# Kernel tuning notes

Measured on AMD Instinct MI355X. Metric: run time of the kernel, lower is better.

The kernel has to match this reference:

```python
import jax, jax.numpy as jnp
import numpy as np

N = 100000
E = 1600000
IN_F = 16
OUT_F = 16
HEADS = 6
ALPHA_COEFF = 0.2
NEG_SLOPE = 0.2


def setup_inputs() -> dict:
    key = jax.random.key(0)
    k1, k2, k3, k4, k5, k6 = jax.random.split(key, 6)
    data = jax.random.uniform(k1, (N, IN_F), dtype=jnp.float32)
    edge_index = jax.random.randint(k2, (2, E), 0, N, dtype=jnp.int64)
    # GATConv params (glorot-ish scale)
    W = jax.random.normal(k3, (IN_F, HEADS * OUT_F), dtype=jnp.float32) * (1.0 / np.sqrt(IN_F))
    att_src = jax.random.normal(k4, (1, HEADS, OUT_F), dtype=jnp.float32) * (1.0 / np.sqrt(OUT_F))
    att_dst = jax.random.normal(k5, (1, HEADS, OUT_F), dtype=jnp.float32) * (1.0 / np.sqrt(OUT_F))
    bias = jnp.zeros((OUT_F,), dtype=jnp.float32)
    return {"data": data, "edge_index": edge_index, "W": W,
            "att_src": att_src, "att_dst": att_dst, "bias": bias}


def _gat_deformer(data, edge_index, W, att_src, att_dst, bias):
    n = data.shape[0]
    # add self loops (PyG GATConv default add_self_loops=True)
    loop = jnp.arange(n, dtype=edge_index.dtype)
    src = jnp.concatenate([edge_index[0], loop])  # [E']
    dst = jnp.concatenate([edge_index[1], loop])  # [E']

    x = (data @ W).reshape(n, HEADS, OUT_F)          # [N,H,C]
    a_src = jnp.sum(x * att_src, axis=-1)            # [N,H]
    a_dst = jnp.sum(x * att_dst, axis=-1)            # [N,H]

    e = a_src[src] + a_dst[dst]                      # [E',H]
    e = jnp.where(e > 0, e, NEG_SLOPE * e)           # leaky_relu(0.2)
    # segment softmax over destination nodes (PyG softmax, +1e-16 denom)
    seg_max = jax.ops.segment_max(e, dst, num_segments=n)
    e = jnp.exp(e - seg_max[dst])
    seg_sum = jax.ops.segment_sum(e, dst, num_segments=n)
    alpha = e / (seg_sum[dst] + 1e-16)               # [E',H]

    # first pass: weighted scatter-add of transformed features
    out = jax.ops.segment_sum(x[src] * alpha[:, :, None], dst, num_segments=n)  # [N,H,C]
    feat = out.mean(axis=1) + bias                   # concat=False -> head mean, + bias

    # second propagate: reuse (scaled) attention on raw coordinates
    coord = data[:, :2]                              # [N,2]
    alpha2 = alpha * ALPHA_COEFF                     # [E',H]
    msg = coord[src][:, None, :] * alpha2[:, :, None]  # [E',H,2]
    out_coord = jax.ops.segment_sum(msg, dst, num_segments=n).mean(axis=1)  # [N,2]

    # fix boundary nodes (masks computed from input coords)
    up = data[:, 0] == 1.0
    down = data[:, 0] == 0.0
    left = data[:, 1] == 0.0
    right = data[:, 1] == 1.0
    c0 = jnp.where(up, 1.0, jnp.where(down, 0.0, out_coord[:, 0]))
    c1 = jnp.where(right, 1.0, jnp.where(left, 0.0, out_coord[:, 1]))
    out_coord = jnp.stack([c0, c1], axis=1)

    feat = jax.nn.selu(feat)
    return out_coord, feat


def reference(data, edge_index, W, att_src, att_dst, bias):
    return _gat_deformer(data, edge_index, W, att_src, att_dst, bias)
```

## Files before the change

### kernel.cpp

```cpp
#include <hip/hip_runtime.h>
#include <hip/hip_fp16.h>
#include <math.h>

#define N_NODES 100000
#define N_EDGES 1600000
#define E_TOT (N_EDGES + N_NODES)
#define IN_FEAT 16
#define OUT_FEAT 16
#define HEADS 6
#define HF 96

#define NB 4096
#define NPB 25
#define CAP 576
#define NBLK_PART 256
#define NT_BLOCKS ((N_NODES * HEADS + 255) / 256)

__global__ void init_cursors(int* __restrict__ gcursor) {
    int b = blockIdx.x * blockDim.x + threadIdx.x;
    if (b < NB) gcursor[b] = b * CAP;
}

__global__ void prep(const int* __restrict__ esrc,
                     const int* __restrict__ edst,
                     int* __restrict__ gcursor,
                     unsigned int* __restrict__ spack,
                     const float* __restrict__ data,
                     const float* __restrict__ W,
                     const float* __restrict__ att_src,
                     const float* __restrict__ att_dst,
                     float* __restrict__ a_src,
                     float* __restrict__ a_dst,
                     unsigned short* __restrict__ data_f16) {
    __shared__ int shmem[2 * NB];

    if (blockIdx.x < NBLK_PART) {
        int* hist = shmem;
        int* base = shmem + NB;
        const int chunk = (E_TOT + NBLK_PART - 1) / NBLK_PART;
        const int e0 = blockIdx.x * chunk;
        const int e1 = min(e0 + chunk, E_TOT);

        for (int j = threadIdx.x; j < NB; j += blockDim.x) hist[j] = 0;
        __syncthreads();
        for (int e = e0 + threadIdx.x; e < e1; e += blockDim.x) {
            int d = (e < N_EDGES) ? edst[e] : (e - N_EDGES);
            atomicAdd(&hist[d / NPB], 1);
        }
        __syncthreads();
        for (int j = threadIdx.x; j < NB; j += blockDim.x) {
            int c = hist[j];
            base[j] = c ? atomicAdd(&gcursor[j], c) : 0;
        }
        __syncthreads();
        for (int j = threadIdx.x; j < NB; j += blockDim.x) hist[j] = 0;
        __syncthreads();
        for (int e = e0 + threadIdx.x; e < e1; e += blockDim.x) {
            int s, d;
            if (e < N_EDGES) { s = esrc[e]; d = edst[e]; }
            else             { s = d = e - N_EDGES; }
            int b = d / NPB;
            int r = atomicAdd(&hist[b], 1);
            int pos = base[b] + r;
            if (pos < (b + 1) * CAP)
                spack[pos] = (unsigned int)s | ((unsigned int)(d - b * NPB) << 17);
        }
    } else {
        float* sW  = (float*)shmem;
        float* sAs = sW + IN_FEAT * HF;
        float* sAd = sAs + HF;
        for (int i = threadIdx.x; i < IN_FEAT * HF; i += blockDim.x) sW[i] = W[i];
        for (int i = threadIdx.x; i < HF; i += blockDim.x) { sAs[i] = att_src[i]; sAd[i] = att_dst[i]; }
        __syncthreads();

        int gid = (blockIdx.x - NBLK_PART) * blockDim.x + threadIdx.x;
        int n = gid / HEADS;
        int h = gid % HEADS;
        if (n >= N_NODES) return;

        float dv[IN_FEAT];
        const float4* dp = (const float4*)(data + (size_t)n * IN_FEAT);
#pragma unroll
        for (int q = 0; q < 4; q++) {
            float4 v = dp[q];
            dv[q*4+0] = v.x; dv[q*4+1] = v.y; dv[q*4+2] = v.z; dv[q*4+3] = v.w;
        }

        if (h < 4) {
            unsigned int lo = (unsigned int)__half_as_ushort(__float2half_rn(dv[h*4+0]))
                            | ((unsigned int)__half_as_ushort(__float2half_rn(dv[h*4+1])) << 16);
            unsigned int hi = (unsigned int)__half_as_ushort(__float2half_rn(dv[h*4+2]))
                            | ((unsigned int)__half_as_ushort(__float2half_rn(dv[h*4+3])) << 16);
            uint2 pk; pk.x = lo; pk.y = hi;
            *(uint2*)(data_f16 + (size_t)n * IN_FEAT + h * 4) = pk;
        }

        float outv[OUT_FEAT];
#pragma unroll
        for (int fo = 0; fo < OUT_FEAT; fo++) outv[fo] = 0.f;
#pragma unroll
        for (int k = 0; k < IN_FEAT; k++) {
            float dk = dv[k];
            const float* wrow = &sW[k * HF + h * OUT_FEAT];
#pragma unroll
            for (int fo = 0; fo < OUT_FEAT; fo++) outv[fo] = fmaf(dk, wrow[fo], outv[fo]);
        }

        float as = 0.f, ad = 0.f;
#pragma unroll
        for (int fo = 0; fo < OUT_FEAT; fo++) {
            as = fmaf(outv[fo], sAs[h * OUT_FEAT + fo], as);
            ad = fmaf(outv[fo], sAd[h * OUT_FEAT + fo], ad);
        }
        a_src[n * HEADS + h] = as;
        a_dst[n * HEADS + h] = ad;
    }
}

__global__ void bucket_accumulate(const int* __restrict__ gcursor,
                                  const unsigned int* __restrict__ spack,
                                  const float* __restrict__ data,
                                  const unsigned short* __restrict__ data_f16,
                                  const float* __restrict__ a_src,
                                  const float* __restrict__ a_dst,
                                  const float* __restrict__ W,
                                  const float* __restrict__ bias,
                                  float* __restrict__ out) {
    const int b = blockIdx.x;
    const int n0 = b * NPB;
    if (n0 >= N_NODES) return;
    const int nn = min(NPB, N_NODES - n0);

    __shared__ unsigned int olist[CAP];
    __shared__ unsigned short exl[CAP * 8];
    __shared__ float wsn_l[NPB * 100];
    __shared__ int cnt[NPB];
    __shared__ int start[NPB + 1];
    __shared__ int cur[NPB];

    const int tid  = threadIdx.x;
    const int lane = tid & 63;
    const int slot = lane >> 4;
    const int f    = lane & 15;
    const int wv   = tid >> 6;

    int ecnt = gcursor[b] - b * CAP;
    if (ecnt > CAP) ecnt = CAP;

    for (int j = tid; j < NPB; j += 256) cnt[j] = 0;
    __syncthreads();
    for (int i = tid; i < ecnt; i += 256)
        atomicAdd(&cnt[spack[b * CAP + i] >> 17], 1);
    __syncthreads();
    if (tid == 0) {
        int r = 0;
        for (int j = 0; j < NPB; j++) { start[j] = r; r += cnt[j]; }
        start[NPB] = r;
    }
    __syncthreads();
    for (int j = tid; j < NPB; j += 256) cur[j] = start[j];
    __syncthreads();
    for (int i = tid; i < ecnt; i += 256) {
        unsigned int p = spack[b * CAP + i];
        int dl = (int)(p >> 17);
        int pos = atomicAdd(&cur[dl], 1);
        olist[pos] = p;
    }
    __syncthreads();

    for (int idx = tid; idx < ecnt * 8; idx += 256) {
        int i = idx >> 3, h = idx & 7;
        if (h < HEADS) {
            unsigned int p = olist[i];
            int s  = (int)(p & 0x1FFFFu);
            int dl = (int)(p >> 17);
            float e = a_src[s * HEADS + h] + a_dst[(n0 + dl) * HEADS + h];
            e = e > 0.f ? e : 0.2f * e;
            exl[i * 8 + h] = __half_as_ushort(__float2half_rn(__expf(e)));
        }
    }
    __syncthreads();

    for (int dl = wv; dl < nn; dl += 4) {
        const int s0 = start[dl];
        const int s1 = s0 + cnt[dl];

        float ws[HEADS], dn[HEADS];
#pragma unroll
        for (int h = 0; h < HEADS; h++) { ws[h] = 0.f; dn[h] = 0.f; }

        for (int pos = s0 + slot; pos < s1; pos += 4) {
            int s = (int)(olist[pos] & 0x1FFFFu);
            float dv = __half2float(__ushort_as_half(data_f16[(size_t)s * IN_FEAT + f]));
            uint4 e4 = *(const uint4*)(exl + pos * 8);
            float ex0 = __half2float(__ushort_as_half((unsigned short)(e4.x & 0xFFFFu)));
            float ex1 = __half2float(__ushort_as_half((unsigned short)(e4.x >> 16)));
            float ex2 = __half2float(__ushort_as_half((unsigned short)(e4.y & 0xFFFFu)));
            float ex3 = __half2float(__ushort_as_half((unsigned short)(e4.y >> 16)));
            float ex4 = __half2float(__ushort_as_half((unsigned short)(e4.z & 0xFFFFu)));
            float ex5 = __half2float(__ushort_as_half((unsigned short)(e4.z >> 16)));
            ws[0] = fmaf(dv, ex0, ws[0]); dn[0] += ex0;
            ws[1] = fmaf(dv, ex1, ws[1]); dn[1] += ex1;
            ws[2] = fmaf(dv, ex2, ws[2]); dn[2] += ex2;
            ws[3] = fmaf(dv, ex3, ws[3]); dn[3] += ex3;
            ws[4] = fmaf(dv, ex4, ws[4]); dn[4] += ex4;
            ws[5] = fmaf(dv, ex5, ws[5]); dn[5] += ex5;
        }

#pragma unroll
        for (int h = 0; h < HEADS; h++) {
            ws[h] += __shfl_xor(ws[h], 16, 64);
            ws[h] += __shfl_xor(ws[h], 32, 64);
            dn[h] += __shfl_xor(dn[h], 16, 64);
            dn[h] += __shfl_xor(dn[h], 32, 64);
        }

        if (slot == 0) {
            float cs = 0.f;
#pragma unroll
            for (int h = 0; h < HEADS; h++) {
                float wsn = ws[h] * __builtin_amdgcn_rcpf(dn[h] + 1e-16f);
                cs += wsn;
                wsn_l[dl * 100 + h * 16 + f] = wsn;
            }
            if (f < 2) {
                float c = cs * (0.2f / 6.f);
                float key = data[(size_t)(n0 + dl) * IN_FEAT + f];
                if (key == 1.0f)      c = 1.0f;
                else if (key == 0.0f) c = 0.0f;
                out[(n0 + dl) * 2 + f] = c;
            }
        }
    }
    __syncthreads();

    const float sc = 1.0507009873554805f;
    const float al = 1.6732632423543772f;
    for (int task = tid; task < nn * 16; task += 256) {
        int dl = task >> 4, fo = task & 15;
        float acc = 0.f;
#pragma unroll
        for (int h = 0; h < HEADS; h++) {
            const float* wr = wsn_l + dl * 100 + h * 16;
            const float* Wc = W + h * 16 + fo;
#pragma unroll
            for (int k = 0; k < IN_FEAT; k++)
                acc = fmaf(wr[k], Wc[k * HF], acc);
        }
        float v = acc * (1.f / 6.f) + bias[fo];
        v = v > 0.f ? sc * v : sc * al * (__expf(v) - 1.f);
        out[2 * N_NODES + (size_t)(n0 + dl) * OUT_FEAT + fo] = v;
    }
}

extern "C" void kernel_launch(void* const* d_in, const int* in_sizes, int n_in,
                              void* d_out, int out_size, void* d_ws, size_t ws_size,
                              hipStream_t stream) {
    const float* data    = (const float*)d_in[0];
    const int*   eidx    = (const int*)d_in[1];
    const float* W       = (const float*)d_in[2];
    const float* att_src = (const float*)d_in[3];
    const float* att_dst = (const float*)d_in[4];
    const float* bias    = (const float*)d_in[5];
    float*       out     = (float*)d_out;
    float*       ws      = (float*)d_ws;

    float*          a_src    = ws;
    float*          a_dst    = ws + 600000;
    int*            gcursor  = (int*)(ws + 1200000);
    unsigned int*   spack    = (unsigned int*)(ws + 1204096);
    unsigned short* data_f16 = (unsigned short*)(ws + 3563392);

    init_cursors<<<(NB + 255) / 256, 256, 0, stream>>>(gcursor);

    prep<<<NBLK_PART + NT_BLOCKS, 256, 0, stream>>>(
        eidx, eidx + N_EDGES, gcursor, spack,
        data, W, att_src, att_dst, a_src, a_dst, data_f16);

    bucket_accumulate<<<NB, 256, 0, stream>>>(
        gcursor, spack, data, data_f16, a_src, a_dst, W, bias, out);
}
```

Before: 159.9 us.

## Use fixed-degree per-node slots and compute attention exps inline with dynamic node scheduling

Result: slower. 194.6 us (+21.8%).

```diff
diff --git a/kernel.cpp b/kernel.cpp
--- a/kernel.cpp
+++ b/kernel.cpp
@@ -11,15 +11,12 @@
 #define HF 96
 
 #define NB 4096
+#define NBA 4000
 #define NPB 25
 #define CAP 576
+#define MAXDEG 64
 #define NBLK_PART 256
 #define NT_BLOCKS ((N_NODES * HEADS + 255) / 256)
-
-__global__ void init_cursors(int* __restrict__ gcursor) {
-    int b = blockIdx.x * blockDim.x + threadIdx.x;
-    if (b < NB) gcursor[b] = b * CAP;
-}
 
 __global__ void prep(const int* __restrict__ esrc,
                      const int* __restrict__ edst,
@@ -61,7 +58,7 @@
             else             { s = d = e - N_EDGES; }
             int b = d / NPB;
             int r = atomicAdd(&hist[b], 1);
-            int pos = base[b] + r;
+            int pos = b * CAP + base[b] + r;
             if (pos < (b + 1) * CAP)
                 spack[pos] = (unsigned int)s | ((unsigned int)(d - b * NPB) << 17);
         }
@@ -117,102 +114,82 @@
     }
 }
 
-__global__ void bucket_accumulate(const int* __restrict__ gcursor,
-                                  const unsigned int* __restrict__ spack,
-                                  const float* __restrict__ data,
-                                  const unsigned short* __restrict__ data_f16,
-                                  const float* __restrict__ a_src,
-                                  const float* __restrict__ a_dst,
-                                  const float* __restrict__ W,
-                                  const float* __restrict__ bias,
-                                  float* __restrict__ out) {
+__global__ __launch_bounds__(256, 8)
+void bucket_accumulate(const int* __restrict__ gcursor,
+                       const unsigned int* __restrict__ spack,
+                       const float* __restrict__ data,
+                       const unsigned short* __restrict__ data_f16,
+                       const float* __restrict__ a_src,
+                       const float* __restrict__ a_dst,
+                       const float* __restrict__ W,
+                       const float* __restrict__ bias,
+                       float* __restrict__ out) {
     const int b = blockIdx.x;
     const int n0 = b * NPB;
-    if (n0 >= N_NODES) return;
-    const int nn = min(NPB, N_NODES - n0);
-
-    __shared__ unsigned int olist[CAP];
-    __shared__ unsigned short exl[CAP * 8];
+    __shared__ unsigned int olist[NPB * MAXDEG];
     __shared__ float wsn_l[NPB * 100];
     __shared__ int cnt[NPB];
-    __shared__ int start[NPB + 1];
-    __shared__ int cur[NPB];
+    __shared__ int nidx;
 
     const int tid  = threadIdx.x;
     const int lane = tid & 63;
     const int slot = lane >> 4;
     const int f    = lane & 15;
-    const int wv   = tid >> 6;
-
-    int ecnt = gcursor[b] - b * CAP;
+
+    int ecnt = gcursor[b];
     if (ecnt > CAP) ecnt = CAP;
 
     for (int j = tid; j < NPB; j += 256) cnt[j] = 0;
+    if (tid == 0) nidx = 0;
     __syncthreads();
-    for (int i = tid; i < ecnt; i += 256)
-        atomicAdd(&cnt[spack[b * CAP + i] >> 17], 1);
-    __syncthreads();
-    if (tid == 0) {
-        int r = 0;
-        for (int j = 0; j < NPB; j++) { start[j] = r; r += cnt[j]; }
-        start[NPB] = r;
-    }
-    __syncthreads();
-    for (int j = tid; j < NPB; j += 256) cur[j] = start[j];
-    __syncthreads();
+
     for (int i = tid; i < ecnt; i += 256) {
         unsigned int p = spack[b * CAP + i];
         int dl = (int)(p >> 17);
-        int pos = atomicAdd(&cur[dl], 1);
-        olist[pos] = p;
+        int r = atomicAdd(&cnt[dl], 1);
+        if (r < MAXDEG)
+            olist[dl * MAXDEG + r] = p & 0x1FFFFu;
     }
     __syncthreads();
 
-    for (int idx = tid; idx < ecnt * 8; idx += 256) {
-        int i = idx >> 3, h = idx & 7;
-        if (h < HEADS) {
-            unsigned int p = olist[i];
-            int s  = (int)(p & 0x1FFFFu);
-            int dl = (int)(p >> 17);
-            float e = a_src[s * HEADS + h] + a_dst[(n0 + dl) * HEADS + h];
-            e = e > 0.f ? e : 0.2f * e;
-            exl[i * 8 + h] = __half_as_ushort(__float2half_rn(__expf(e)));
-        }
-    }
-    __syncthreads();
-
-    for (int dl = wv; dl < nn; dl += 4) {
-        const int s0 = start[dl];
-        const int s1 = s0 + cnt[dl];
+    for (;;) {
+        int my;
+        if (lane == 0) my = atomicAdd(&nidx, 1);
+        my = __builtin_amdgcn_readfirstlane(my);
+        if (my >= NPB) break;
+        const int n = n0 + my;
+
+        float ad[HEADS];
+#pragma unroll
+        for (int h = 0; h < HEADS; h++) ad[h] = a_dst[n * HEADS + h];
+
+        int T = cnt[my];
+        if (T > MAXDEG) T = MAXDEG;
+        const unsigned int* ol = olist + my * MAXDEG;
 
         float ws[HEADS], dn[HEADS];
 #pragma unroll
         for (int h = 0; h < HEADS; h++) { ws[h] = 0.f; dn[h] = 0.f; }
 
-        for (int pos = s0 + slot; pos < s1; pos += 4) {
-            int s = (int)(olist[pos] & 0x1FFFFu);
+        for (int t = slot; t < T; t += 4) {
+            int s = (int)ol[t];
             float dv = __half2float(__ushort_as_half(data_f16[(size_t)s * IN_FEAT + f]));
-            uint4 e4 = *(const uint4*)(exl + pos * 8);
-            float ex0 = __half2float(__ushort_as_half((unsigned short)(e4.x & 0xFFFFu)));
-            float ex1 = __half2float(__ushort_as_half((unsigned short)(e4.x >> 16)));
-            float ex2 = __half2float(__ushort_as_half((unsigned short)(e4.y & 0xFFFFu)));
-            float ex3 = __half2float(__ushort_as_half((unsigned short)(e4.y >> 16)));
-            float ex4 = __half2float(__ushort_as_half((unsigned short)(e4.z & 0xFFFFu)));
-            float ex5 = __half2float(__ushort_as_half((unsigned short)(e4.z >> 16)));
-            ws[0] = fmaf(dv, ex0, ws[0]); dn[0] += ex0;
-            ws[1] = fmaf(dv, ex1, ws[1]); dn[1] += ex1;
-            ws[2] = fmaf(dv, ex2, ws[2]); dn[2] += ex2;
-            ws[3] = fmaf(dv, ex3, ws[3]); dn[3] += ex3;
-            ws[4] = fmaf(dv, ex4, ws[4]); dn[4] += ex4;
-            ws[5] = fmaf(dv, ex5, ws[5]); dn[5] += ex5;
+#pragma unroll
+            for (int h = 0; h < HEADS; h++) {
+                float e = a_src[s * HEADS + h] + ad[h];
+                e = e > 0.f ? e : 0.2f * e;
+                float ex = __expf(e);
+                ws[h] = fmaf(dv, ex, ws[h]);
+                dn[h] += ex;
+            }
         }
 
 #pragma unroll
         for (int h = 0; h < HEADS; h++) {
-            ws[h] += __shfl_xor(ws[h], 16, 64);
-            ws[h] += __shfl_xor(ws[h], 32, 64);
-            dn[h] += __shfl_xor(dn[h], 16, 64);
-            dn[h] += __shfl_xor(dn[h], 32, 64);
+            ws[h] += __shfl_xor(ws[h], 16);
+            ws[h] += __shfl_xor(ws[h], 32);
+            dn[h] += __shfl_xor(dn[h], 16);
+            dn[h] += __shfl_xor(dn[h], 32);
         }
 
         if (slot == 0) {
@@ -221,14 +198,14 @@
             for (int h = 0; h < HEADS; h++) {
                 float wsn = ws[h] * __builtin_amdgcn_rcpf(dn[h] + 1e-16f);
                 cs += wsn;
-                wsn_l[dl * 100 + h * 16 + f] = wsn;
+                wsn_l[my * 100 + h * 16 + f] = wsn;
             }
             if (f < 2) {
                 float c = cs * (0.2f / 6.f);
-                float key = data[(size_t)(n0 + dl) * IN_FEAT + f];
+                float key = data[(size_t)n * IN_FEAT + f];
                 if (key == 1.0f)      c = 1.0f;
                 else if (key == 0.0f) c = 0.0f;
-                out[(n0 + dl) * 2 + f] = c;
+                out[n * 2 + f] = c;
             }
         }
     }
@@ -236,7 +213,7 @@
 
     const float sc = 1.0507009873554805f;
     const float al = 1.6732632423543772f;
-    for (int task = tid; task < nn * 16; task += 256) {
+    for (int task = tid; task < NPB * 16; task += 256) {
         int dl = task >> 4, fo = task & 15;
         float acc = 0.f;
 #pragma unroll
@@ -271,12 +248,12 @@
     unsigned int*   spack    = (unsigned int*)(ws + 1204096);
     unsigned short* data_f16 = (unsigned short*)(ws + 3563392);
 
-    init_cursors<<<(NB + 255) / 256, 256, 0, stream>>>(gcursor);
+    hipMemsetAsync(gcursor, 0, NB * sizeof(int), stream);
 
     prep<<<NBLK_PART + NT_BLOCKS, 256, 0, stream>>>(
         eidx, eidx + N_EDGES, gcursor, spack,
         data, W, att_src, att_dst, a_src, a_dst, data_f16);
 
-    bucket_accumulate<<<NB, 256, 0, stream>>>(
+    bucket_accumulate<<<NBA, 256, 0, stream>>>(
         gcursor, spack, data, data_f16, a_src, a_dst, W, bias, out);
 }
```
